# Kernel tuning notes

Hardware: AMD Instinct MI355X
Metric: run time of the kernel (lower is better)

## Reference

```python
import jax, jax.numpy as jnp
import numpy as np

ALIGNED_H, ALIGNED_W, ALIGNED_T = 7, 7, 4
SPATIAL_SCALE, TIME_SCALE = 1.0 / 16.0, 1.0
B, C, T, H, W = 4, 256, 16, 64, 64
N_ROIS = 1200


def setup_inputs() -> dict:
    key = jax.random.key(0)
    kf, kb, kx, ky, kw, kh, kt, kd = jax.random.split(key, 8)
    features = jax.random.normal(kf, (B, C, T, H, W), dtype=jnp.float32)
    b = jax.random.randint(kb, (N_ROIS,), 0, B).astype(jnp.float32)
    # image-space boxes (1024x1024 image, stride-16 features); temporal interval in frame units
    x1 = jax.random.uniform(kx, (N_ROIS,), minval=0.0, maxval=700.0)
    y1 = jax.random.uniform(ky, (N_ROIS,), minval=0.0, maxval=700.0)
    x2 = jnp.minimum(x1 + jax.random.uniform(kw, (N_ROIS,), minval=32.0, maxval=320.0), 1023.0)
    y2 = jnp.minimum(y1 + jax.random.uniform(kh, (N_ROIS,), minval=32.0, maxval=320.0), 1023.0)
    t1 = jax.random.uniform(kt, (N_ROIS,), minval=0.0, maxval=10.0)
    t2 = jnp.minimum(t1 + jax.random.uniform(kd, (N_ROIS,), minval=2.0, maxval=6.0), 15.0)
    rois = jnp.stack([b, x1, y1, x2, y2, t1, t2], axis=1)  # [N, 7]
    return {"features": features, "rois": rois}


def _axis_samples(start, end, size, n_out):
    # classic roi_align sampling: bin = (end - start + 1) / (n_out - 1), sample at start + i*bin
    length = jnp.maximum(end - start + 1.0, 1.0)                                  # [N]
    step = length / (n_out - 1.0)
    coord = start[:, None] + step[:, None] * jnp.arange(n_out, dtype=jnp.float32)[None, :]  # [N, n_out]
    valid = (coord >= 0.0) & (coord < size)
    lo = jnp.clip(jnp.floor(coord), 0.0, size - 1.0)
    frac = coord - lo
    lo_i = lo.astype(jnp.int32)
    hi_i = jnp.minimum(lo_i + 1, size - 1)
    return lo_i, hi_i, frac, valid.astype(jnp.float32)


def roi_align_3d(features, rois, p_t, p_h, p_w, sscale, tscale):
    Bf, Cf, Tf, Hf, Wf = features.shape
    f = jnp.transpose(features, (0, 2, 3, 4, 1))  # [B,T,H,W,C] channel-last for clean gather
    bidx = rois[:, 0].astype(jnp.int32)
    x1 = rois[:, 1] * sscale
    y1 = rois[:, 2] * sscale
    x2 = rois[:, 3] * sscale
    y2 = rois[:, 4] * sscale
    t1 = rois[:, 5] * tscale
    t2 = rois[:, 6] * tscale
    tl, th, tfr, tv = _axis_samples(t1, t2, Tf, p_t)  # [N, p_t]
    yl, yh, yfr, yv = _axis_samples(y1, y2, Hf, p_h)  # [N, p_h]
    xl, xh, xfr, xv = _axis_samples(x1, x2, Wf, p_w)  # [N, p_w]
    b4 = bidx[:, None, None, None]
    out = jnp.zeros((rois.shape[0], p_t, p_h, p_w, Cf), dtype=features.dtype)
    # trilinear interpolation: sum over 8 corners
    for ti, wt in ((tl, 1.0 - tfr), (th, tfr)):
        for yi, wy in ((yl, 1.0 - yfr), (yh, yfr)):
            for xi, wx in ((xl, 1.0 - xfr), (xh, xfr)):
                v = f[b4, ti[:, :, None, None], yi[:, None, :, None], xi[:, None, None, :]]  # [N,pt,ph,pw,C]
                w = wt[:, :, None, None] * wy[:, None, :, None] * wx[:, None, None, :]
                out = out + v * w[..., None]
    # zero out-of-bounds sample points (matches CUDA kernel behavior)
    mask = tv[:, :, None, None] * yv[:, None, :, None] * xv[:, None, None, :]
    out = out * mask[..., None]
    return jnp.transpose(out, (0, 4, 1, 2, 3))  # [N, C, p_t, p_h, p_w]


def _avg_pool3d_k2s1(x):
    s = x[..., :-1, :, :] + x[..., 1:, :, :]
    s = s[..., :, :-1, :] + s[..., :, 1:, :]
    s = s[..., :, :, :-1] + s[..., :, :, 1:]
    return s * 0.125


def reference(features, rois):
    x = roi_align_3d(features, rois, ALIGNED_T + 1, ALIGNED_H + 1, ALIGNED_W + 1,
                     SPATIAL_SCALE, TIME_SCALE)
    return _avg_pool3d_k2s1(x)  # [N, C, ALIGNED_T, ALIGNED_H, ALIGNED_W]
```

## Files before the change

kernel.cpp:

```cpp
#include <hip/hip_runtime.h>

#define C_ 256
#define T_ 16
#define H_ 64
#define W_ 64
#define PT 5
#define PH 8
#define PW 8
#define OT 4
#define OH 7
#define OW 7
#define SSCALE (1.0f/16.0f)
#define TSCALE 1.0f
#define CG 32
#define LROW 66
#define NOUT (CG * OT * OH * OW)

typedef float f4v __attribute__((ext_vector_type(4)));
typedef float f2v __attribute__((ext_vector_type(2)));
typedef _Float16 h2v __attribute__((ext_vector_type(2)));
typedef _Float16 h8v __attribute__((ext_vector_type(8)));

__global__ __launch_bounds__(256) void transpose_kernel(const float* __restrict__ f,
                                                        _Float16* __restrict__ ft) {
    __shared__ unsigned tile[64 * 128];
    const int THW = T_ * H_ * W_;
    int thw0 = blockIdx.x * 64;
    int b = blockIdx.y;
    int q = threadIdx.x & 15;
    int cp0 = threadIdx.x >> 4;

#pragma unroll
    for (int k = 0; k < 8; ++k) {
        int cp = k * 16 + cp0;
        int c = cp * 2;
        const f4v* s0 = reinterpret_cast<const f4v*>(
            &f[((size_t)b * C_ + c) * THW + thw0 + q * 4]);
        const f4v* s1 = reinterpret_cast<const f4v*>(
            &f[((size_t)b * C_ + c + 1) * THW + thw0 + q * 4]);
        f4v va = __builtin_nontemporal_load(s0);
        f4v vb = __builtin_nontemporal_load(s1);
#pragma unroll
        for (int j = 0; j < 4; ++j) {
            int row = q * 4 + j;
            h2v hp = {(_Float16)va[j], (_Float16)vb[j]};
            tile[row * 128 + (cp ^ (row & 30))] = __builtin_bit_cast(unsigned, hp);
        }
    }
    __syncthreads();

    int wv = threadIdx.x >> 6;
    int ln = threadIdx.x & 63;
    size_t orow = ((size_t)b * THW + thw0) * C_;
#pragma unroll
    for (int i = 0; i < 16; ++i) {
        int row = wv * 16 + i;
        int s = row & 30;
        uint2 w = *reinterpret_cast<const uint2*>(&tile[row * 128 + ((ln * 2) ^ s)]);
        *reinterpret_cast<uint2*>(&ft[orow + (size_t)row * C_ + ln * 4]) = w;
    }
}

__global__ __launch_bounds__(1024) void sort_rois(const float* __restrict__ rois,
                                                  int nroi, int* __restrict__ perm) {
    __shared__ unsigned key[2048];
    int t = threadIdx.x;
    if (nroi > 2048) {
        for (int i = t; i < nroi; i += 1024) perm[i] = i;
        return;
    }
    for (int i = t; i < 2048; i += 1024) {
        unsigned k = 0x1FFFFFu;
        if (i < nroi) {
            const float* rp = rois + i * 7;
            int bb = (int)rp[0];
            float xc = (rp[1] + rp[3]) * 0.5f * SSCALE;
            float yc = (rp[2] + rp[4]) * 0.5f * SSCALE;
            float tc = (rp[5] + rp[6]) * 0.5f * TSCALE;
            int xq = min(63, max(0, (int)xc));
            int yq = min(63, max(0, (int)yc));
            int tq = min(15, max(0, (int)tc));
            unsigned m = 0;
#pragma unroll
            for (int bit = 0; bit < 6; ++bit)
                m |= (((yq >> bit) & 1u) << (2 * bit + 1)) |
                     (((xq >> bit) & 1u) << (2 * bit));
            k = ((((unsigned)bb << 12) | m) << 4) | (unsigned)tq;
        }
        key[i] = (k << 11) | (unsigned)i;
    }
    __syncthreads();
    for (int kk = 2; kk <= 2048; kk <<= 1) {
        for (int j = kk >> 1; j > 0; j >>= 1) {
            for (int i = t; i < 2048; i += 1024) {
                int ixj = i ^ j;
                if (ixj > i) {
                    unsigned a = key[i], c = key[ixj];
                    bool up = (i & kk) == 0;
                    if ((a > c) == up) { key[i] = c; key[ixj] = a; }
                }
            }
            __syncthreads();
        }
    }
    for (int i = t; i < 2048; i += 1024)
        if (i < nroi) perm[i] = (int)(key[i] & 0x7FFu);
}

__global__ __launch_bounds__(256) void roi_kernel(const _Float16* __restrict__ ft,
                                                  const float* __restrict__ rois,
                                                  const int* __restrict__ perm,
                                                  float* __restrict__ out) {
    __shared__ float scratch[NOUT];
    __shared__ float sroi[7];
    __shared__ int2 s_trow[PT]; __shared__ float2 s_twt[PT];
    __shared__ int2 s_yrow[PH]; __shared__ float2 s_ywt[PH];
    __shared__ int2 s_xoff[PW]; __shared__ float2 s_xwt[PW];

    int bid = blockIdx.x;
    int r = perm[bid >> 3];
    int cg = bid & 7;
    int c0 = cg * CG;

    if (threadIdx.x < 7) sroi[threadIdx.x] = rois[r * 7 + threadIdx.x];
    __syncthreads();

    if (threadIdx.x < 21) {
        int i = threadIdx.x;
        float start, end, size;
        int j, n, scale;
        if (i < 5) {
            j = i; n = PT;
            start = sroi[5] * TSCALE; end = sroi[6] * TSCALE;
            size = (float)T_; scale = H_ * W_ * C_ * 2;
        } else if (i < 13) {
            j = i - 5; n = PH;
            start = sroi[2] * SSCALE; end = sroi[4] * SSCALE;
            size = (float)H_; scale = W_ * C_ * 2;
        } else {
            j = i - 13; n = PW;
            start = sroi[1] * SSCALE; end = sroi[3] * SSCALE;
            size = (float)W_; scale = C_ * 2;
        }
        float length = fmaxf(end - start + 1.0f, 1.0f);
        float step = length / (float)(n - 1);
        float coord = start + step * (float)j;
        float valid = (coord >= 0.0f && coord < size) ? 1.0f : 0.0f;
        float lo = fminf(fmaxf(floorf(coord), 0.0f), size - 1.0f);
        int lo_i = (int)lo;
        int hi_i = min(lo_i + 1, (int)size - 1);
        float fr = coord - lo;
        int2 offs; offs.x = lo_i * scale; offs.y = hi_i * scale;
        float2 wts; wts.x = (1.0f - fr) * valid; wts.y = fr * valid;
        if (i < 5)       { s_trow[j] = offs; s_twt[j] = wts; }
        else if (i < 13) { s_yrow[j] = offs; s_ywt[j] = wts; }
        else             { s_xoff[j] = offs; s_xwt[j] = wts; }
    }
    __syncthreads();

    int b = (int)sroi[0];
    int c4 = threadIdx.x & 3;
    int slot = threadIdx.x >> 2;
    const char* fb = (const char*)ft
        + ((size_t)b * (T_ * H_ * W_ * C_) + (size_t)(c0 + c4 * 8)) * 2;

    float (*buf)[LROW] = (float(*)[LROW])scratch;
    int cc = threadIdx.x & 31;
    int hh = threadIdx.x >> 5;

    float racc[OT][OW];
#pragma unroll
    for (int t = 0; t < OT; ++t)
#pragma unroll
        for (int w = 0; w < OW; ++w) racc[t][w] = 0.0f;

    int y = slot >> 3, x = slot & 7;
    int2 yr = s_yrow[y]; float2 yw = s_ywt[y];
    int2 xo = s_xoff[x]; float2 xw = s_xwt[x];

#pragma unroll
    for (int t = 0; t < PT; ++t) {
        if (t) __syncthreads();

        int2 tr = s_trow[t];
        float2 tw = s_twt[t];
        int rA = tr.x + yr.x;
        int rB = tr.x + yr.y;
        int rC = tr.y + yr.x;
        int rD = tr.y + yr.y;
        float wA = tw.x * yw.x, wB = tw.x * yw.y;
        float wC = tw.y * yw.x, wD = tw.y * yw.y;

        f4v accL = {0.f, 0.f, 0.f, 0.f};
        f4v accH = {0.f, 0.f, 0.f, 0.f};
#pragma unroll
        for (int tap = 0; tap < 8; ++tap) {
            int ro = (tap & 1) ? ((tap >> 1) == 0 ? rA : (tap >> 1) == 1 ? rB
                                  : (tap >> 1) == 2 ? rC : rD) + xo.y
                               : ((tap >> 1) == 0 ? rA : (tap >> 1) == 1 ? rB
                                  : (tap >> 1) == 2 ? rC : rD) + xo.x;
            float w = ((tap >> 1) == 0 ? wA : (tap >> 1) == 1 ? wB
                       : (tap >> 1) == 2 ? wC : wD) * ((tap & 1) ? xw.y : xw.x);
            h8v h = *(const h8v*)(fb + ro);
            f4v lo = {(float)h[0], (float)h[1], (float)h[2], (float)h[3]};
            f4v hi = {(float)h[4], (float)h[5], (float)h[6], (float)h[7]};
            accL += w * lo;
            accH += w * hi;
        }
        {
            float* col = &buf[c4 * 8][slot];
            col[0 * LROW] = accL[0];
            col[1 * LROW] = accL[1];
            col[2 * LROW] = accL[2];
            col[3 * LROW] = accL[3];
            col[4 * LROW] = accH[0];
            col[5 * LROW] = accH[1];
            col[6 * LROW] = accH[2];
            col[7 * LROW] = accH[3];
        }
        __syncthreads();

        if (hh < 7) {
            const float* p = &buf[cc][hh * 8];
            float p2[8];
#pragma unroll
            for (int x2 = 0; x2 < 4; ++x2) {
                f2v a = *(const f2v*)(p + 2 * x2);
                f2v bq = *(const f2v*)(p + 8 + 2 * x2);
                f2v s = a + bq;
                p2[2 * x2] = s[0];
                p2[2 * x2 + 1] = s[1];
            }
#pragma unroll
            for (int w = 0; w < OW; ++w) {
                float pw = p2[w] + p2[w + 1];
                if (t < OT) racc[t][w] += pw;
                if (t > 0) racc[t - 1][w] += pw;
            }
        }
    }
    __syncthreads();

    if (hh < 7) {
        int base = cc * (OT * OH * OW) + hh * OW;
#pragma unroll
        for (int t = 0; t < OT; ++t)
#pragma unroll
            for (int w = 0; w < OW; ++w)
                scratch[base + t * (OH * OW) + w] = racc[t][w] * 0.125f;
    }
    __syncthreads();

    float* outb = out + ((size_t)r * C_ + c0) * (OT * OH * OW);
    const f4v* s4 = (const f4v*)scratch;
    f4v* o4 = (f4v*)outb;
    for (int k = 0; k < 7; ++k) {
        int idx = k * 256 + threadIdx.x;
        if (idx < NOUT / 4) __builtin_nontemporal_store(s4[idx], &o4[idx]);
    }
}

__device__ __forceinline__ void axis_sample(float start, float end, float size, int n,
                                            int j, int& lo_i, int& hi_i, float& frac,
                                            float& valid) {
    float length = fmaxf(end - start + 1.0f, 1.0f);
    float step = length / (float)(n - 1);
    float coord = start + step * (float)j;
    valid = (coord >= 0.0f && coord < size) ? 1.0f : 0.0f;
    float lo = fminf(fmaxf(floorf(coord), 0.0f), size - 1.0f);
    frac = coord - lo;
    lo_i = (int)lo;
    hi_i = min(lo_i + 1, (int)size - 1);
}

__global__ void roi_direct(const float* __restrict__ f, const float* __restrict__ rois,
                           float* __restrict__ out, long long total) {
    long long idx = (long long)blockIdx.x * 256 + threadIdx.x;
    if (idx >= total) return;
    int w = (int)(idx % OW);
    long long q = idx / OW;
    int h = (int)(q % OH);
    q /= OH;
    int t = (int)(q % OT);
    q /= OT;
    int c = (int)(q % C_);
    int r = (int)(q / C_);

    float rb = rois[r * 7 + 0];
    float x1 = rois[r * 7 + 1] * SSCALE;
    float y1 = rois[r * 7 + 2] * SSCALE;
    float x2 = rois[r * 7 + 3] * SSCALE;
    float y2 = rois[r * 7 + 4] * SSCALE;
    float t1 = rois[r * 7 + 5] * TSCALE;
    float t2 = rois[r * 7 + 6] * TSCALE;
    int b = (int)rb;
    const float* fc = f + ((size_t)b * C_ + c) * (T_ * H_ * W_);

    float acc = 0.0f;
    for (int dt = 0; dt < 2; ++dt) {
        int tlo, thi; float tf, tv;
        axis_sample(t1, t2, (float)T_, PT, t + dt, tlo, thi, tf, tv);
        for (int dh = 0; dh < 2; ++dh) {
            int ylo, yhi; float yf, yv;
            axis_sample(y1, y2, (float)H_, PH, h + dh, ylo, yhi, yf, yv);
            for (int dw = 0; dw < 2; ++dw) {
                int xlo, xhi; float xf, xv;
                axis_sample(x1, x2, (float)W_, PW, w + dw, xlo, xhi, xf, xv);
                float v000 = fc[(tlo * H_ + ylo) * W_ + xlo];
                float v001 = fc[(tlo * H_ + ylo) * W_ + xhi];
                float v010 = fc[(tlo * H_ + yhi) * W_ + xlo];
                float v011 = fc[(tlo * H_ + yhi) * W_ + xhi];
                float v100 = fc[(thi * H_ + ylo) * W_ + xlo];
                float v101 = fc[(thi * H_ + ylo) * W_ + xhi];
                float v110 = fc[(thi * H_ + yhi) * W_ + xlo];
                float v111 = fc[(thi * H_ + yhi) * W_ + xhi];
                float vx00 = v000 + xf * (v001 - v000);
                float vx01 = v010 + xf * (v011 - v010);
                float vx10 = v100 + xf * (v101 - v100);
                float vx11 = v110 + xf * (v111 - v110);
                float vy0 = vx00 + yf * (vx01 - vx00);
                float vy1 = vx10 + yf * (vx11 - vx10);
                float v = vy0 + tf * (vy1 - vy0);
                acc += v * (tv * yv * xv);
            }
        }
    }
    out[idx] = acc * 0.125f;
}

extern "C" void kernel_launch(void* const* d_in, const int* in_sizes, int n_in,
                              void* d_out, int out_size, void* d_ws, size_t ws_size,
                              hipStream_t stream) {
    const float* feat = (const float*)d_in[0];
    const float* rois = (const float*)d_in[1];
    float* out = (float*)d_out;
    int nroi = in_sizes[1] / 7;
    int B = in_sizes[0] / (C_ * T_ * H_ * W_);
    size_t ftbytes = (size_t)B * T_ * H_ * W_ * C_ * sizeof(_Float16);
    size_t need = ftbytes + 2048 * sizeof(int);

    if (ws_size >= need && nroi >= 1) {
        _Float16* ft = (_Float16*)d_ws;
        int* perm = (int*)((char*)d_ws + ftbytes);
        sort_rois<<<1, 1024, 0, stream>>>(rois, nroi, perm);
        dim3 g1(T_ * H_ * W_ / 64, B);
        transpose_kernel<<<g1, 256, 0, stream>>>(feat, ft);
        roi_kernel<<<dim3(nroi * (C_ / CG)), 256, 0, stream>>>(ft, rois, perm, out);
    } else {
        long long total = (long long)nroi * C_ * OT * OH * OW;
        roi_direct<<<(int)((total + 255) / 256), 256, 0, stream>>>(feat, rois, out, total);
    }
}
```

Measured before the change: 525.3 us.

## Prefetch next time-slice gathers into registers and double-buffer the LDS pooling plane

```diff
diff --git a/kernel.cpp b/kernel.cpp
--- a/kernel.cpp
+++ b/kernel.cpp
@@ -14,12 +14,22 @@
 #define TSCALE 1.0f
 #define CG 32
 #define LROW 66
+#define PLN (CG * LROW)
 #define NOUT (CG * OT * OH * OW)
 
 typedef float f4v __attribute__((ext_vector_type(4)));
 typedef float f2v __attribute__((ext_vector_type(2)));
 typedef _Float16 h2v __attribute__((ext_vector_type(2)));
 typedef _Float16 h8v __attribute__((ext_vector_type(8)));
+
+__device__ __forceinline__ f4v lo4(h8v h) {
+    f4v r = {(float)h[0], (float)h[1], (float)h[2], (float)h[3]};
+    return r;
+}
+__device__ __forceinline__ f4v hi4(h8v h) {
+    f4v r = {(float)h[4], (float)h[5], (float)h[6], (float)h[7]};
+    return r;
+}
 
 __global__ __launch_bounds__(256) void transpose_kernel(const float* __restrict__ f,
                                                         _Float16* __restrict__ ft) {
@@ -107,10 +117,10 @@
         if (i < nroi) perm[i] = (int)(key[i] & 0x7FFu);
 }
 
-__global__ __launch_bounds__(256) void roi_kernel(const _Float16* __restrict__ ft,
-                                                  const float* __restrict__ rois,
-                                                  const int* __restrict__ perm,
-                                                  float* __restrict__ out) {
+__global__ __launch_bounds__(256, 4) void roi_kernel(const _Float16* __restrict__ ft,
+                                                     const float* __restrict__ rois,
+                                                     const int* __restrict__ perm,
+                                                     float* __restrict__ out) {
     __shared__ float scratch[NOUT];
     __shared__ float sroi[7];
     __shared__ int2 s_trow[PT]; __shared__ float2 s_twt[PT];
@@ -164,7 +174,7 @@
     const char* fb = (const char*)ft
         + ((size_t)b * (T_ * H_ * W_ * C_) + (size_t)(c0 + c4 * 8)) * 2;
 
-    float (*buf)[LROW] = (float(*)[LROW])scratch;
+    float* bufs[2] = {scratch, scratch + PLN};
     int cc = threadIdx.x & 31;
     int hh = threadIdx.x >> 5;
 
@@ -177,51 +187,66 @@
     int y = slot >> 3, x = slot & 7;
     int2 yr = s_yrow[y]; float2 yw = s_ywt[y];
     int2 xo = s_xoff[x]; float2 xw = s_xwt[x];
+    int o00 = yr.x + xo.x, o01 = yr.x + xo.y;
+    int o10 = yr.y + xo.x, o11 = yr.y + xo.y;
+
+    h8v cur[8], nxt[8];
+    {
+        int2 tr = s_trow[0];
+        cur[0] = *(const h8v*)(fb + tr.x + o00);
+        cur[1] = *(const h8v*)(fb + tr.x + o01);
+        cur[2] = *(const h8v*)(fb + tr.x + o10);
+        cur[3] = *(const h8v*)(fb + tr.x + o11);
+        cur[4] = *(const h8v*)(fb + tr.y + o00);
+        cur[5] = *(const h8v*)(fb + tr.y + o01);
+        cur[6] = *(const h8v*)(fb + tr.y + o10);
+        cur[7] = *(const h8v*)(fb + tr.y + o11);
+    }
 
 #pragma unroll
     for (int t = 0; t < PT; ++t) {
-        if (t) __syncthreads();
-
-        int2 tr = s_trow[t];
+        if (t + 1 < PT) {
+            int2 tr = s_trow[t + 1];
+            nxt[0] = *(const h8v*)(fb + tr.x + o00);
+            nxt[1] = *(const h8v*)(fb + tr.x + o01);
+            nxt[2] = *(const h8v*)(fb + tr.x + o10);
+            nxt[3] = *(const h8v*)(fb + tr.x + o11);
+            nxt[4] = *(const h8v*)(fb + tr.y + o00);
+            nxt[5] = *(const h8v*)(fb + tr.y + o01);
+            nxt[6] = *(const h8v*)(fb + tr.y + o10);
+            nxt[7] = *(const h8v*)(fb + tr.y + o11);
+        }
+
         float2 tw = s_twt[t];
-        int rA = tr.x + yr.x;
-        int rB = tr.x + yr.y;
-        int rC = tr.y + yr.x;
-        int rD = tr.y + yr.y;
-        float wA = tw.x * yw.x, wB = tw.x * yw.y;
-        float wC = tw.y * yw.x, wD = tw.y * yw.y;
-
-        f4v accL = {0.f, 0.f, 0.f, 0.f};
-        f4v accH = {0.f, 0.f, 0.f, 0.f};
-#pragma unroll
-        for (int tap = 0; tap < 8; ++tap) {
-            int ro = (tap & 1) ? ((tap >> 1) == 0 ? rA : (tap >> 1) == 1 ? rB
-                                  : (tap >> 1) == 2 ? rC : rD) + xo.y
-                               : ((tap >> 1) == 0 ? rA : (tap >> 1) == 1 ? rB
-                                  : (tap >> 1) == 2 ? rC : rD) + xo.x;
-            float w = ((tap >> 1) == 0 ? wA : (tap >> 1) == 1 ? wB
-                       : (tap >> 1) == 2 ? wC : wD) * ((tap & 1) ? xw.y : xw.x);
-            h8v h = *(const h8v*)(fb + ro);
-            f4v lo = {(float)h[0], (float)h[1], (float)h[2], (float)h[3]};
-            f4v hi = {(float)h[4], (float)h[5], (float)h[6], (float)h[7]};
-            accL += w * lo;
-            accH += w * hi;
-        }
+        f4v vx00L = xw.x * lo4(cur[0]) + xw.y * lo4(cur[1]);
+        f4v vx01L = xw.x * lo4(cur[2]) + xw.y * lo4(cur[3]);
+        f4v vx10L = xw.x * lo4(cur[4]) + xw.y * lo4(cur[5]);
+        f4v vx11L = xw.x * lo4(cur[6]) + xw.y * lo4(cur[7]);
+        f4v vx00H = xw.x * hi4(cur[0]) + xw.y * hi4(cur[1]);
+        f4v vx01H = xw.x * hi4(cur[2]) + xw.y * hi4(cur[3]);
+        f4v vx10H = xw.x * hi4(cur[4]) + xw.y * hi4(cur[5]);
+        f4v vx11H = xw.x * hi4(cur[6]) + xw.y * hi4(cur[7]);
+        f4v vL = tw.x * (yw.x * vx00L + yw.y * vx01L)
+               + tw.y * (yw.x * vx10L + yw.y * vx11L);
+        f4v vH = tw.x * (yw.x * vx00H + yw.y * vx01H)
+               + tw.y * (yw.x * vx10H + yw.y * vx11H);
+
+        float* bp = bufs[t & 1];
         {
-            float* col = &buf[c4 * 8][slot];
-            col[0 * LROW] = accL[0];
-            col[1 * LROW] = accL[1];
-            col[2 * LROW] = accL[2];
-            col[3 * LROW] = accL[3];
-            col[4 * LROW] = accH[0];
-            col[5 * LROW] = accH[1];
-            col[6 * LROW] = accH[2];
-            col[7 * LROW] = accH[3];
+            float* col = &bp[(c4 * 8) * LROW + slot];
+            col[0 * LROW] = vL[0];
+            col[1 * LROW] = vL[1];
+            col[2 * LROW] = vL[2];
+            col[3 * LROW] = vL[3];
+            col[4 * LROW] = vH[0];
+            col[5 * LROW] = vH[1];
+            col[6 * LROW] = vH[2];
+            col[7 * LROW] = vH[3];
         }
         __syncthreads();
 
         if (hh < 7) {
-            const float* p = &buf[cc][hh * 8];
+            const float* p = &bp[cc * LROW + hh * 8];
             float p2[8];
 #pragma unroll
             for (int x2 = 0; x2 < 4; ++x2) {
@@ -238,6 +263,9 @@
                 if (t > 0) racc[t - 1][w] += pw;
             }
         }
+
+#pragma unroll
+        for (int i = 0; i < 8; ++i) cur[i] = nxt[i];
     }
     __syncthreads();
 
```

New measurement: 524.2 us. Within noise of the previous version (-0.2%).
